# Performance work log

Measured on AMD Instinct MI355X. Metric: run time of the kernel, lower is better.

## Reference

```python
import jax, jax.numpy as jnp
import numpy as np

B, D, U = 8192, 1024, 1024


def setup_inputs() -> dict:
    key = jax.random.key(0)
    ks = jax.random.split(key, 11)
    scale = 0.05  # keras 'random_normal' initializer default stddev
    inp = {
        "inputs": jax.random.normal(ks[0], (B, D), jnp.float32),
        "h_tm1": jax.random.normal(ks[1], (B, U), jnp.float32),
        "c_tm1": jax.random.normal(ks[2], (B, U), jnp.float32),
        "W_i": jax.random.normal(ks[3], (D, U), jnp.float32) * scale,
        "U_i": jax.random.normal(ks[4], (U, U), jnp.float32) * scale,
        "b_i": jnp.zeros((U,), jnp.float32),
        "W_f": jax.random.normal(ks[5], (D, U), jnp.float32) * scale,
        "U_f": jax.random.normal(ks[6], (U, U), jnp.float32) * scale,
        "b_f": jnp.zeros((U,), jnp.float32),
        "W_c": jax.random.normal(ks[7], (D, U), jnp.float32) * scale,
        "U_c": jax.random.normal(ks[8], (U, U), jnp.float32) * scale,
        "b_c": jnp.zeros((U,), jnp.float32),
        "W_o": jax.random.normal(ks[9], (D, U), jnp.float32) * scale,
        "U_o": jax.random.normal(ks[10], (U, U), jnp.float32) * scale,
        "b_o": jnp.zeros((U,), jnp.float32),
    }
    return inp


def reference(inputs, h_tm1, c_tm1, W_i, U_i, b_i, W_f, U_f, b_f, W_c, U_c, b_c, W_o, U_o, b_o):
    # Concatenate the 4 gate projections into single GEMMs (same math, fused form)
    Wx = jnp.concatenate([W_i, W_f, W_c, W_o], axis=1)  # [D, 4U]
    Uh = jnp.concatenate([U_i, U_f, U_c, U_o], axis=1)  # [U, 4U]
    b = jnp.concatenate([b_i, b_f, b_c, b_o], axis=0)   # [4U]
    z = inputs @ Wx + h_tm1 @ Uh + b                     # [B, 4U]
    u = W_i.shape[1]
    zi, zf, zc, zo = z[:, :u], z[:, u:2 * u], z[:, 2 * u:3 * u], z[:, 3 * u:]
    i = jax.nn.sigmoid(zi)
    f = jax.nn.sigmoid(zf)
    c_ = jnp.tanh(zc)
    c = f * c_tm1 + i * c_
    o = jax.nn.sigmoid(zo)
    h = o * jnp.tanh(c)
    return (h, c)
```

## Files before the change

### kernel.cpp

```cpp
#include <hip/hip_runtime.h>
#include <hip/hip_bf16.h>
#include <cstdint>


using f32x4  = __attribute__((ext_vector_type(4))) float;
using short8 = __attribute__((ext_vector_type(8))) short;

__device__ __forceinline__ unsigned short f2bf(float f) {
  union { float f; unsigned int u; } v; v.f = f;
  unsigned int r = v.u + 0x7fffu + ((v.u >> 16) & 1u);
  return (unsigned short)(r >> 16);
}
__device__ __forceinline__ float sigmoidf_fast(float x) { return 1.f / (1.f + __expf(-x)); }
__device__ __forceinline__ float tanhf_fast(float x)    { return 1.f - 2.f / (__expf(2.f * x) + 1.f); }

__global__ void conv_a_kernel(const float* __restrict__ X, const float* __restrict__ H,
                              unsigned short* __restrict__ Abf) {
  int idx = blockIdx.x * blockDim.x + threadIdx.x;
  int b  = idx >> 8;
  int kq = (idx & 255) << 2;
  float4 x = *(const float4*)(X + (long)b * 1024 + kq);
  float4 h = *(const float4*)(H + (long)b * 1024 + kq);
  ushort4 xo, ho;
  xo.x = f2bf(x.x); xo.y = f2bf(x.y); xo.z = f2bf(x.z); xo.w = f2bf(x.w);
  ho.x = f2bf(h.x); ho.y = f2bf(h.y); ho.z = f2bf(h.z); ho.w = f2bf(h.w);
  *(ushort4*)(Abf + (long)b * 2048 + kq)        = xo;
  *(ushort4*)(Abf + (long)b * 2048 + 1024 + kq) = ho;
}

__global__ void conv_b_kernel(const float* W_i, const float* U_i,
                              const float* W_f, const float* U_f,
                              const float* W_c, const float* U_c,
                              const float* W_o, const float* U_o,
                              unsigned short* __restrict__ Bt) {
  __shared__ float tile[64][65];
  int z = blockIdx.z;
  const float* src;
  switch (z) {
    case 0: src = W_i; break; case 1: src = U_i; break;
    case 2: src = W_f; break; case 3: src = U_f; break;
    case 4: src = W_c; break; case 5: src = U_c; break;
    case 6: src = W_o; break; default: src = U_o; break;
  }
  int g = z >> 1, s = z & 1;
  int k0 = blockIdx.x * 64;
  int u0 = blockIdx.y * 64;
  int t = threadIdx.x;
  int c = t & 63, r0 = t >> 6;
#pragma unroll
  for (int i = 0; i < 16; ++i) {
    int r = i * 4 + r0;
    tile[r][c] = src[(long)(k0 + r) * 1024 + u0 + c];
  }
  __syncthreads();
  int ul = t >> 2;
  int ks = (t & 3) * 16;
  unsigned short outv[16];
#pragma unroll
  for (int j = 0; j < 16; ++j) outv[j] = f2bf(tile[ks + j][ul]);
  long n   = 4L * u0 + (ul >> 4) * 64 + g * 16 + (ul & 15);
  long col = (long)s * 1024 + k0 + ks;
  uint4* dst = (uint4*)(Bt + n * 2048 + col);
  dst[0] = *(uint4*)(outv);
  dst[1] = *(uint4*)(outv + 8);
}

__global__ __launch_bounds__(512, 2) void lstm_gemm_kernel(
    const unsigned short* __restrict__ Abf,
    const unsigned short* __restrict__ Btbf,
    const float* __restrict__ b_i, const float* __restrict__ b_f,
    const float* __restrict__ b_c, const float* __restrict__ b_o,
    const float* __restrict__ c_tm1,
    float* __restrict__ outH, float* __restrict__ outC) {
  __shared__ unsigned short smem[49152];

  int bid = blockIdx.x;
  int swz = (bid & 7) * 64 + (bid >> 3);
  int bm = swz >> 4;
  int bn = swz & 15;

  int t = threadIdx.x;
  int lane = t & 63;
  int w = t >> 6;
  int wm = w >> 2;
  int wn = w & 3;
  int rl = lane & 15;
  int kg = lane >> 4;

#define AOFFE(MI) ((wm * 128 + (MI) * 16 + rl) * 32 + \
    ((kg ^ (((wm * 128 + (MI) * 16 + rl) >> 1) & 3)) << 3))
#define BOFFE(NI) (8192 + (wn * 64 + (NI) * 16 + rl) * 32 + \
    ((kg ^ (((wn * 64 + (NI) * 16 + rl) >> 1) & 3)) << 3))
  const int offA0 = AOFFE(0), offA1 = AOFFE(1), offA2 = AOFFE(2), offA3 = AOFFE(3);
  const int offA4 = AOFFE(4), offA5 = AOFFE(5), offA6 = AOFFE(6), offA7 = AOFFE(7);
  const int offB0 = BOFFE(0), offB1 = BOFFE(1), offB2 = BOFFE(2), offB3 = BOFFE(3);
#undef AOFFE
#undef BOFFE

  int srow = t >> 2;
  int cbe  = (((t & 3) ^ ((srow >> 1) & 3))) << 3;
  const unsigned short* aS0 = Abf  + (long)(bm * 256 + srow) * 2048 + cbe;
  const unsigned short* aS1 = aS0 + 128L * 2048;
  const unsigned short* bS0 = Btbf + (long)(bn * 256 + srow) * 2048 + cbe;
  const unsigned short* bS1 = bS0 + 128L * 2048;
  const int dA = t * 8;

#define GLL(SRC, DELM)                                                                     \
  __builtin_amdgcn_global_load_lds((const __attribute__((address_space(1))) void*)(SRC),   \
      (__attribute__((address_space(3))) void*)(&smem[DELM]), 16, 0, 0)
#define VMC(N) asm volatile("s_waitcnt vmcnt(" #N ")" ::: "memory")

  f32x4 acc[8][4];
#pragma unroll
  for (int mi = 0; mi < 8; ++mi)
#pragma unroll
    for (int ni = 0; ni < 4; ++ni) acc[mi][ni] = (f32x4){0.f, 0.f, 0.f, 0.f};

  short8 aw0, aw1, aw2, aw3, bb0, bb1, bb2, bb3;

#define MF4(AF, MI)                                                                      \
  acc[MI][0] = __builtin_amdgcn_mfma_f32_16x16x32_bf16(AF, bb0, acc[MI][0], 0, 0, 0);    \
  acc[MI][1] = __builtin_amdgcn_mfma_f32_16x16x32_bf16(AF, bb1, acc[MI][1], 0, 0, 0);    \
  acc[MI][2] = __builtin_amdgcn_mfma_f32_16x16x32_bf16(AF, bb2, acc[MI][2], 0, 0, 0);    \
  acc[MI][3] = __builtin_amdgcn_mfma_f32_16x16x32_bf16(AF, bb3, acc[MI][3], 0, 0, 0);

#define WINDOW(RB, SB, KOFF, DOSTAGE, VMN, DOBAR)                              \
  {                                                                            \
    const unsigned short* Ab_ = smem + (RB) * 16384;                           \
    bb0 = *(const short8*)(Ab_ + offB0);                                       \
    bb1 = *(const short8*)(Ab_ + offB1);                                       \
    bb2 = *(const short8*)(Ab_ + offB2);                                       \
    bb3 = *(const short8*)(Ab_ + offB3);                                       \
    aw0 = *(const short8*)(Ab_ + offA0);                                       \
    aw1 = *(const short8*)(Ab_ + offA1);                                       \
    aw2 = *(const short8*)(Ab_ + offA2);                                       \
    aw3 = *(const short8*)(Ab_ + offA3);                                       \
    if (DOSTAGE) {                                                             \
      GLL(aS0 + (KOFF), (SB) * 16384 + dA);                                    \
      GLL(aS1 + (KOFF), (SB) * 16384 + 4096 + dA);                             \
    }                                                                          \
    __builtin_amdgcn_s_setprio(1);                                             \
    MF4(aw0, 0) MF4(aw1, 1) MF4(aw2, 2) MF4(aw3, 3)                            \
    __builtin_amdgcn_s_setprio(0);                                             \
    aw0 = *(const short8*)(Ab_ + offA4);                                       \
    aw1 = *(const short8*)(Ab_ + offA5);                                       \
    aw2 = *(const short8*)(Ab_ + offA6);                                       \
    aw3 = *(const short8*)(Ab_ + offA7);                                       \
    if (DOSTAGE) {                                                             \
      GLL(bS0 + (KOFF), (SB) * 16384 + 8192 + dA);                             \
      GLL(bS1 + (KOFF), (SB) * 16384 + 12288 + dA);                            \
    }                                                                          \
    __builtin_amdgcn_s_setprio(1);                                             \
    MF4(aw0, 4) MF4(aw1, 5) MF4(aw2, 6) MF4(aw3, 7)                            \
    __builtin_amdgcn_s_setprio(0);                                             \
    if ((VMN) == 4) VMC(4);                                                    \
    if ((VMN) == 0) VMC(0);                                                    \
    if (DOBAR) __builtin_amdgcn_s_barrier();                                   \
  }

  GLL(aS0, dA);            GLL(aS1, 4096 + dA);
  GLL(bS0, 8192 + dA);     GLL(bS1, 12288 + dA);
  GLL(aS0 + 32, 16384 + dA);        GLL(aS1 + 32, 16384 + 4096 + dA);
  GLL(bS0 + 32, 16384 + 8192 + dA); GLL(bS1 + 32, 16384 + 12288 + dA);
  VMC(4);
  __builtin_amdgcn_s_barrier();
  aS0 += 64; aS1 += 64; bS0 += 64; bS1 += 64;

  for (int g = 0; g < 20; ++g) {
    WINDOW(0, 2, 0,  1, 4, 1);
    WINDOW(1, 0, 32, 1, 4, 1);
    WINDOW(2, 1, 64, 1, 4, 1);
    aS0 += 96; aS1 += 96; bS0 += 96; bS1 += 96;
  }
  WINDOW(0, 2, 0,  1, 4, 1);
  WINDOW(1, 0, 32, 1, 4, 1);
  WINDOW(2, 0, 0,  0, 0, 1);
  WINDOW(0, 0, 0,  0, -1, 0);
#undef WINDOW
#undef MF4
#undef VMC
#undef GLL

  int mbase = bm * 256 + wm * 128;
  int nbase = bn * 256 + wn * 64;
  int u = (nbase >> 2) + rl;
  float bi_v = b_i[u], bf_v = b_f[u], bc_v = b_c[u], bo_v = b_o[u];
  int rquad = (lane >> 4) << 2;
#pragma unroll
  for (int mi = 0; mi < 8; ++mi) {
#pragma unroll
    for (int j = 0; j < 4; ++j) {
      int brow = mbase + mi * 16 + rquad + j;
      float zi = acc[mi][0][j] + bi_v;
      float zf = acc[mi][1][j] + bf_v;
      float zc = acc[mi][2][j] + bc_v;
      float zo = acc[mi][3][j] + bo_v;
      float ig = sigmoidf_fast(zi);
      float fg = sigmoidf_fast(zf);
      float cg = tanhf_fast(zc);
      float og = sigmoidf_fast(zo);
      float cp = c_tm1[(long)brow * 1024 + u];
      float cn = fg * cp + ig * cg;
      float hn = og * tanhf_fast(cn);
      outH[(long)brow * 1024 + u] = hn;
      outC[(long)brow * 1024 + u] = cn;
    }
  }
}

extern "C" void kernel_launch(void* const* d_in, const int* in_sizes, int n_in,
                              void* d_out, int out_size, void* d_ws, size_t ws_size,
                              hipStream_t stream) {
  (void)in_sizes; (void)n_in; (void)out_size; (void)ws_size;
  const float* X   = (const float*)d_in[0];
  const float* Hst = (const float*)d_in[1];
  const float* Cst = (const float*)d_in[2];
  const float* W_i = (const float*)d_in[3];
  const float* U_i = (const float*)d_in[4];
  const float* b_i = (const float*)d_in[5];
  const float* W_f = (const float*)d_in[6];
  const float* U_f = (const float*)d_in[7];
  const float* b_f = (const float*)d_in[8];
  const float* W_c = (const float*)d_in[9];
  const float* U_c = (const float*)d_in[10];
  const float* b_c = (const float*)d_in[11];
  const float* W_o = (const float*)d_in[12];
  const float* U_o = (const float*)d_in[13];
  const float* b_o = (const float*)d_in[14];

  unsigned short* Abf  = (unsigned short*)d_ws;
  unsigned short* Btbf = (unsigned short*)((char*)d_ws + 33554432);

  float* outH = (float*)d_out;
  float* outC = outH + 8192L * 1024;

  conv_a_kernel<<<8192, 256, 0, stream>>>(X, Hst, Abf);
  conv_b_kernel<<<dim3(16, 16, 8), 256, 0, stream>>>(W_i, U_i, W_f, U_f, W_c, U_c, W_o, U_o, Btbf);
  lstm_gemm_kernel<<<512, 512, 0, stream>>>(Abf, Btbf, b_i, b_f, b_c, b_o, Cst, outH, outC);
}
```

Baseline: 159.7 us.

## Load A fragments directly from global into registers, stage only B in LDS

After: 335.3 us. +109.9%, slower.

```diff
diff --git a/kernel.cpp b/kernel.cpp
--- a/kernel.cpp
+++ b/kernel.cpp
@@ -72,7 +72,7 @@
     const float* __restrict__ b_c, const float* __restrict__ b_o,
     const float* __restrict__ c_tm1,
     float* __restrict__ outH, float* __restrict__ outC) {
-  __shared__ unsigned short smem[49152];
+  __shared__ unsigned short smem[3 * 8192];
 
   int bid = blockIdx.x;
   int swz = (bid & 7) * 64 + (bid >> 3);
@@ -87,27 +87,27 @@
   int rl = lane & 15;
   int kg = lane >> 4;
 
-#define AOFFE(MI) ((wm * 128 + (MI) * 16 + rl) * 32 + \
-    ((kg ^ (((wm * 128 + (MI) * 16 + rl) >> 1) & 3)) << 3))
-#define BOFFE(NI) (8192 + (wn * 64 + (NI) * 16 + rl) * 32 + \
+#define BOFFE(NI) ((wn * 64 + (NI) * 16 + rl) * 32 + \
     ((kg ^ (((wn * 64 + (NI) * 16 + rl) >> 1) & 3)) << 3))
-  const int offA0 = AOFFE(0), offA1 = AOFFE(1), offA2 = AOFFE(2), offA3 = AOFFE(3);
-  const int offA4 = AOFFE(4), offA5 = AOFFE(5), offA6 = AOFFE(6), offA7 = AOFFE(7);
   const int offB0 = BOFFE(0), offB1 = BOFFE(1), offB2 = BOFFE(2), offB3 = BOFFE(3);
-#undef AOFFE
 #undef BOFFE
+
+  const unsigned short* gA = Abf + (long)(bm * 256 + wm * 128 + rl) * 2048 + kg * 8;
 
   int srow = t >> 2;
   int cbe  = (((t & 3) ^ ((srow >> 1) & 3))) << 3;
-  const unsigned short* aS0 = Abf  + (long)(bm * 256 + srow) * 2048 + cbe;
-  const unsigned short* aS1 = aS0 + 128L * 2048;
   const unsigned short* bS0 = Btbf + (long)(bn * 256 + srow) * 2048 + cbe;
   const unsigned short* bS1 = bS0 + 128L * 2048;
-  const int dA = t * 8;
+  const int dB = t * 8;
 
 #define GLL(SRC, DELM)                                                                     \
   __builtin_amdgcn_global_load_lds((const __attribute__((address_space(1))) void*)(SRC),   \
       (__attribute__((address_space(3))) void*)(&smem[DELM]), 16, 0, 0)
+#define GLLB(SB, KOFF)                                                         \
+  do {                                                                         \
+    GLL(bS0 + (KOFF), (SB) * 8192 + dB);                                       \
+    GLL(bS1 + (KOFF), (SB) * 8192 + 4096 + dB);                                \
+  } while (0)
 #define VMC(N) asm volatile("s_waitcnt vmcnt(" #N ")" ::: "memory")
 
   f32x4 acc[8][4];
@@ -116,7 +116,21 @@
 #pragma unroll
     for (int ni = 0; ni < 4; ++ni) acc[mi][ni] = (f32x4){0.f, 0.f, 0.f, 0.f};
 
-  short8 aw0, aw1, aw2, aw3, bb0, bb1, bb2, bb3;
+  short8 pa0, pa1, pa2, pa3, pa4, pa5, pa6, pa7;
+  short8 qa0, qa1, qa2, qa3, qa4, qa5, qa6, qa7;
+  short8 bb0, bb1, bb2, bb3;
+
+#define LOADA(S, KO)                                                           \
+  do {                                                                         \
+    S##a0 = *(const short8*)(gA + 0 * 32768 + (KO));                           \
+    S##a1 = *(const short8*)(gA + 1 * 32768 + (KO));                           \
+    S##a2 = *(const short8*)(gA + 2 * 32768 + (KO));                           \
+    S##a3 = *(const short8*)(gA + 3 * 32768 + (KO));                           \
+    S##a4 = *(const short8*)(gA + 4 * 32768 + (KO));                           \
+    S##a5 = *(const short8*)(gA + 5 * 32768 + (KO));                           \
+    S##a6 = *(const short8*)(gA + 6 * 32768 + (KO));                           \
+    S##a7 = *(const short8*)(gA + 7 * 32768 + (KO));                           \
+  } while (0)
 
 #define MF4(AF, MI)                                                                      \
   acc[MI][0] = __builtin_amdgcn_mfma_f32_16x16x32_bf16(AF, bb0, acc[MI][0], 0, 0, 0);    \
@@ -124,61 +138,48 @@
   acc[MI][2] = __builtin_amdgcn_mfma_f32_16x16x32_bf16(AF, bb2, acc[MI][2], 0, 0, 0);    \
   acc[MI][3] = __builtin_amdgcn_mfma_f32_16x16x32_bf16(AF, bb3, acc[MI][3], 0, 0, 0);
 
-#define WINDOW(RB, SB, KOFF, DOSTAGE, VMN, DOBAR)                              \
+#define WINDOW(RB, SB, KOA, KOB, C, N, DOA, DOST, VMN, DOBAR)                  \
   {                                                                            \
-    const unsigned short* Ab_ = smem + (RB) * 16384;                           \
-    bb0 = *(const short8*)(Ab_ + offB0);                                       \
-    bb1 = *(const short8*)(Ab_ + offB1);                                       \
-    bb2 = *(const short8*)(Ab_ + offB2);                                       \
-    bb3 = *(const short8*)(Ab_ + offB3);                                       \
-    aw0 = *(const short8*)(Ab_ + offA0);                                       \
-    aw1 = *(const short8*)(Ab_ + offA1);                                       \
-    aw2 = *(const short8*)(Ab_ + offA2);                                       \
-    aw3 = *(const short8*)(Ab_ + offA3);                                       \
-    if (DOSTAGE) {                                                             \
-      GLL(aS0 + (KOFF), (SB) * 16384 + dA);                                    \
-      GLL(aS1 + (KOFF), (SB) * 16384 + 4096 + dA);                             \
-    }                                                                          \
+    if (DOA) LOADA(N, KOA);                                                    \
+    const unsigned short* Bb_ = smem + (RB) * 8192;                            \
+    bb0 = *(const short8*)(Bb_ + offB0);                                       \
+    bb1 = *(const short8*)(Bb_ + offB1);                                       \
+    bb2 = *(const short8*)(Bb_ + offB2);                                       \
+    bb3 = *(const short8*)(Bb_ + offB3);                                       \
+    if (DOST) GLLB(SB, KOB);                                                   \
     __builtin_amdgcn_s_setprio(1);                                             \
-    MF4(aw0, 0) MF4(aw1, 1) MF4(aw2, 2) MF4(aw3, 3)                            \
+    MF4(C##a0, 0) MF4(C##a1, 1) MF4(C##a2, 2) MF4(C##a3, 3)                    \
+    MF4(C##a4, 4) MF4(C##a5, 5) MF4(C##a6, 6) MF4(C##a7, 7)                    \
     __builtin_amdgcn_s_setprio(0);                                             \
-    aw0 = *(const short8*)(Ab_ + offA4);                                       \
-    aw1 = *(const short8*)(Ab_ + offA5);                                       \
-    aw2 = *(const short8*)(Ab_ + offA6);                                       \
-    aw3 = *(const short8*)(Ab_ + offA7);                                       \
-    if (DOSTAGE) {                                                             \
-      GLL(bS0 + (KOFF), (SB) * 16384 + 8192 + dA);                             \
-      GLL(bS1 + (KOFF), (SB) * 16384 + 12288 + dA);                            \
-    }                                                                          \
-    __builtin_amdgcn_s_setprio(1);                                             \
-    MF4(aw0, 4) MF4(aw1, 5) MF4(aw2, 6) MF4(aw3, 7)                            \
-    __builtin_amdgcn_s_setprio(0);                                             \
-    if ((VMN) == 4) VMC(4);                                                    \
+    if ((VMN) == 2) VMC(2);                                                    \
     if ((VMN) == 0) VMC(0);                                                    \
     if (DOBAR) __builtin_amdgcn_s_barrier();                                   \
   }
 
-  GLL(aS0, dA);            GLL(aS1, 4096 + dA);
-  GLL(bS0, 8192 + dA);     GLL(bS1, 12288 + dA);
-  GLL(aS0 + 32, 16384 + dA);        GLL(aS1 + 32, 16384 + 4096 + dA);
-  GLL(bS0 + 32, 16384 + 8192 + dA); GLL(bS1 + 32, 16384 + 12288 + dA);
-  VMC(4);
+  GLLB(0, 0);
+  GLLB(1, 32);
+  LOADA(p, 0);
+  VMC(10);
   __builtin_amdgcn_s_barrier();
-  aS0 += 64; aS1 += 64; bS0 += 64; bS1 += 64;
-
-  for (int g = 0; g < 20; ++g) {
-    WINDOW(0, 2, 0,  1, 4, 1);
-    WINDOW(1, 0, 32, 1, 4, 1);
-    WINDOW(2, 1, 64, 1, 4, 1);
-    aS0 += 96; aS1 += 96; bS0 += 96; bS1 += 96;
-  }
-  WINDOW(0, 2, 0,  1, 4, 1);
-  WINDOW(1, 0, 32, 1, 4, 1);
-  WINDOW(2, 0, 0,  0, 0, 1);
-  WINDOW(0, 0, 0,  0, -1, 0);
+
+  for (int g = 0; g < 10; ++g) {
+    WINDOW(0, 2, 32,  64,  p, q, 1, 1, 2, 1);
+    WINDOW(1, 0, 64,  96,  q, p, 1, 1, 2, 1);
+    WINDOW(2, 1, 96,  128, p, q, 1, 1, 2, 1);
+    WINDOW(0, 2, 128, 160, q, p, 1, 1, 2, 1);
+    WINDOW(1, 0, 160, 192, p, q, 1, 1, 2, 1);
+    WINDOW(2, 1, 192, 224, q, p, 1, 1, 2, 1);
+    gA += 192; bS0 += 192; bS1 += 192;
+  }
+  WINDOW(0, 2, 32, 64, p, q, 1, 1, 2, 1);
+  WINDOW(1, 0, 64, 96, q, p, 1, 1, 2, 1);
+  WINDOW(2, 0, 96, 0,  p, q, 1, 0, 0, 1);
+  WINDOW(0, 0, 0,  0,  q, p, 0, 0, -1, 0);
 #undef WINDOW
 #undef MF4
+#undef LOADA
 #undef VMC
+#undef GLLB
 #undef GLL
 
   int mbase = bm * 256 + wm * 128;
```

## Shrink GEMM block tile to 256x128 and raise occupancy to four blocks per CU

Applied to the files above, without the earlier changes.

Result: slower. 174.3 us (+9.1%).

```diff
diff --git a/kernel.cpp b/kernel.cpp
--- a/kernel.cpp
+++ b/kernel.cpp
@@ -65,54 +65,58 @@
   dst[1] = *(uint4*)(outv + 8);
 }
 
-__global__ __launch_bounds__(512, 2) void lstm_gemm_kernel(
+__global__ __launch_bounds__(512, 4) void lstm_gemm_kernel(
     const unsigned short* __restrict__ Abf,
     const unsigned short* __restrict__ Btbf,
     const float* __restrict__ b_i, const float* __restrict__ b_f,
     const float* __restrict__ b_c, const float* __restrict__ b_o,
     const float* __restrict__ c_tm1,
     float* __restrict__ outH, float* __restrict__ outC) {
-  __shared__ unsigned short smem[49152];
+  __shared__ unsigned short smem[3 * 12288];
 
   int bid = blockIdx.x;
-  int swz = (bid & 7) * 64 + (bid >> 3);
-  int bm = swz >> 4;
-  int bn = swz & 15;
+  int swz = (bid & 7) * 128 + (bid >> 3);
+  int bm = swz >> 5;
+  int bn = swz & 31;
 
   int t = threadIdx.x;
   int lane = t & 63;
   int w = t >> 6;
-  int wm = w >> 2;
-  int wn = w & 3;
+  int wm = w >> 1;
+  int wn = w & 1;
   int rl = lane & 15;
   int kg = lane >> 4;
 
-#define AOFFE(MI) ((wm * 128 + (MI) * 16 + rl) * 32 + \
-    ((kg ^ (((wm * 128 + (MI) * 16 + rl) >> 1) & 3)) << 3))
-#define BOFFE(NI) (8192 + (wn * 64 + (NI) * 16 + rl) * 32 + \
+#define AOFFE(MI) (((wm * 64 + (MI) * 16 + rl) * 32) + \
+    ((kg ^ (((wm * 64 + (MI) * 16 + rl) >> 1) & 3)) << 3))
+#define BOFFE(NI) (8192 + ((wn * 64 + (NI) * 16 + rl) * 32) + \
     ((kg ^ (((wn * 64 + (NI) * 16 + rl) >> 1) & 3)) << 3))
   const int offA0 = AOFFE(0), offA1 = AOFFE(1), offA2 = AOFFE(2), offA3 = AOFFE(3);
-  const int offA4 = AOFFE(4), offA5 = AOFFE(5), offA6 = AOFFE(6), offA7 = AOFFE(7);
   const int offB0 = BOFFE(0), offB1 = BOFFE(1), offB2 = BOFFE(2), offB3 = BOFFE(3);
 #undef AOFFE
 #undef BOFFE
 
   int srow = t >> 2;
-  int cbe  = (((t & 3) ^ ((srow >> 1) & 3))) << 3;
+  int cbe  = ((t & 3) ^ ((srow >> 1) & 3)) << 3;
   const unsigned short* aS0 = Abf  + (long)(bm * 256 + srow) * 2048 + cbe;
   const unsigned short* aS1 = aS0 + 128L * 2048;
-  const unsigned short* bS0 = Btbf + (long)(bn * 256 + srow) * 2048 + cbe;
-  const unsigned short* bS1 = bS0 + 128L * 2048;
+  const unsigned short* bS0 = Btbf + (long)(bn * 128 + srow) * 2048 + cbe;
   const int dA = t * 8;
 
 #define GLL(SRC, DELM)                                                                     \
   __builtin_amdgcn_global_load_lds((const __attribute__((address_space(1))) void*)(SRC),   \
       (__attribute__((address_space(3))) void*)(&smem[DELM]), 16, 0, 0)
+#define STAGE(SB, KOFF)                                                        \
+  do {                                                                         \
+    GLL(aS0 + (KOFF), (SB) * 12288 + dA);                                      \
+    GLL(aS1 + (KOFF), (SB) * 12288 + 4096 + dA);                               \
+    GLL(bS0 + (KOFF), (SB) * 12288 + 8192 + dA);                               \
+  } while (0)
 #define VMC(N) asm volatile("s_waitcnt vmcnt(" #N ")" ::: "memory")
 
-  f32x4 acc[8][4];
-#pragma unroll
-  for (int mi = 0; mi < 8; ++mi)
+  f32x4 acc[4][4];
+#pragma unroll
+  for (int mi = 0; mi < 4; ++mi)
 #pragma unroll
     for (int ni = 0; ni < 4; ++ni) acc[mi][ni] = (f32x4){0.f, 0.f, 0.f, 0.f};
 
@@ -126,68 +130,53 @@
 
 #define WINDOW(RB, SB, KOFF, DOSTAGE, VMN, DOBAR)                              \
   {                                                                            \
-    const unsigned short* Ab_ = smem + (RB) * 16384;                           \
-    bb0 = *(const short8*)(Ab_ + offB0);                                       \
-    bb1 = *(const short8*)(Ab_ + offB1);                                       \
-    bb2 = *(const short8*)(Ab_ + offB2);                                       \
-    bb3 = *(const short8*)(Ab_ + offB3);                                       \
-    aw0 = *(const short8*)(Ab_ + offA0);                                       \
-    aw1 = *(const short8*)(Ab_ + offA1);                                       \
-    aw2 = *(const short8*)(Ab_ + offA2);                                       \
-    aw3 = *(const short8*)(Ab_ + offA3);                                       \
-    if (DOSTAGE) {                                                             \
-      GLL(aS0 + (KOFF), (SB) * 16384 + dA);                                    \
-      GLL(aS1 + (KOFF), (SB) * 16384 + 4096 + dA);                             \
-    }                                                                          \
+    const unsigned short* S_ = smem + (RB) * 12288;                            \
+    bb0 = *(const short8*)(S_ + offB0);                                        \
+    bb1 = *(const short8*)(S_ + offB1);                                        \
+    bb2 = *(const short8*)(S_ + offB2);                                        \
+    bb3 = *(const short8*)(S_ + offB3);                                        \
+    aw0 = *(const short8*)(S_ + offA0);                                        \
+    aw1 = *(const short8*)(S_ + offA1);                                        \
+    aw2 = *(const short8*)(S_ + offA2);                                        \
+    aw3 = *(const short8*)(S_ + offA3);                                        \
+    if (DOSTAGE) STAGE(SB, KOFF);                                              \
     __builtin_amdgcn_s_setprio(1);                                             \
     MF4(aw0, 0) MF4(aw1, 1) MF4(aw2, 2) MF4(aw3, 3)                            \
     __builtin_amdgcn_s_setprio(0);                                             \
-    aw0 = *(const short8*)(Ab_ + offA4);                                       \
-    aw1 = *(const short8*)(Ab_ + offA5);                                       \
-    aw2 = *(const short8*)(Ab_ + offA6);                                       \
-    aw3 = *(const short8*)(Ab_ + offA7);                                       \
-    if (DOSTAGE) {                                                             \
-      GLL(bS0 + (KOFF), (SB) * 16384 + 8192 + dA);                             \
-      GLL(bS1 + (KOFF), (SB) * 16384 + 12288 + dA);                            \
-    }                                                                          \
-    __builtin_amdgcn_s_setprio(1);                                             \
-    MF4(aw0, 4) MF4(aw1, 5) MF4(aw2, 6) MF4(aw3, 7)                            \
-    __builtin_amdgcn_s_setprio(0);                                             \
-    if ((VMN) == 4) VMC(4);                                                    \
+    if ((VMN) == 3) VMC(3);                                                    \
     if ((VMN) == 0) VMC(0);                                                    \
     if (DOBAR) __builtin_amdgcn_s_barrier();                                   \
   }
 
-  GLL(aS0, dA);            GLL(aS1, 4096 + dA);
-  GLL(bS0, 8192 + dA);     GLL(bS1, 12288 + dA);
-  GLL(aS0 + 32, 16384 + dA);        GLL(aS1 + 32, 16384 + 4096 + dA);
-  GLL(bS0 + 32, 16384 + 8192 + dA); GLL(bS1 + 32, 16384 + 12288 + dA);
-  VMC(4);
+  STAGE(0, 0);
+  STAGE(1, 32);
+  VMC(3);
   __builtin_amdgcn_s_barrier();
-  aS0 += 64; aS1 += 64; bS0 += 64; bS1 += 64;
+  aS0 += 64; aS1 += 64; bS0 += 64;
 
   for (int g = 0; g < 20; ++g) {
-    WINDOW(0, 2, 0,  1, 4, 1);
-    WINDOW(1, 0, 32, 1, 4, 1);
-    WINDOW(2, 1, 64, 1, 4, 1);
-    aS0 += 96; aS1 += 96; bS0 += 96; bS1 += 96;
-  }
-  WINDOW(0, 2, 0,  1, 4, 1);
-  WINDOW(1, 0, 32, 1, 4, 1);
+    WINDOW(0, 2, 0,  1, 3, 1);
+    WINDOW(1, 0, 32, 1, 3, 1);
+    WINDOW(2, 1, 64, 1, 3, 1);
+    aS0 += 96; aS1 += 96; bS0 += 96;
+  }
+  WINDOW(0, 2, 0,  1, 3, 1);
+  WINDOW(1, 0, 32, 1, 3, 1);
   WINDOW(2, 0, 0,  0, 0, 1);
   WINDOW(0, 0, 0,  0, -1, 0);
 #undef WINDOW
 #undef MF4
 #undef VMC
+#undef STAGE
 #undef GLL
 
-  int mbase = bm * 256 + wm * 128;
-  int nbase = bn * 256 + wn * 64;
+  int mbase = bm * 256 + wm * 64;
+  int nbase = bn * 128 + wn * 64;
   int u = (nbase >> 2) + rl;
   float bi_v = b_i[u], bf_v = b_f[u], bc_v = b_c[u], bo_v = b_o[u];
   int rquad = (lane >> 4) << 2;
 #pragma unroll
-  for (int mi = 0; mi < 8; ++mi) {
+  for (int mi = 0; mi < 4; ++mi) {
 #pragma unroll
     for (int j = 0; j < 4; ++j) {
       int brow = mbase + mi * 16 + rquad + j;
@@ -236,5 +225,5 @@
 
   conv_a_kernel<<<8192, 256, 0, stream>>>(X, Hst, Abf);
   conv_b_kernel<<<dim3(16, 16, 8), 256, 0, stream>>>(W_i, U_i, W_f, U_f, W_c, U_c, W_o, U_o, Btbf);
-  lstm_gemm_kernel<<<512, 512, 0, stream>>>(Abf, Btbf, b_i, b_f, b_c, b_o, Cst, outH, outC);
-}
+  lstm_gemm_kernel<<<1024, 512, 0, stream>>>(Abf, Btbf, b_i, b_f, b_c, b_o, Cst, outH, outC);
+}
```

## Switch GEMM to 32x32x16 MFMA with reshaped warp tiling

Applied to the files above, without the earlier changes.

New measurement: 168.9 us. 1.06x slower.

```diff
diff --git a/kernel.cpp b/kernel.cpp
--- a/kernel.cpp
+++ b/kernel.cpp
@@ -3,7 +3,7 @@
 #include <cstdint>
 
 
-using f32x4  = __attribute__((ext_vector_type(4))) float;
+using f32x16 = __attribute__((ext_vector_type(16))) float;
 using short8 = __attribute__((ext_vector_type(8))) short;
 
 __device__ __forceinline__ unsigned short f2bf(float f) {
@@ -58,7 +58,7 @@
   unsigned short outv[16];
 #pragma unroll
   for (int j = 0; j < 16; ++j) outv[j] = f2bf(tile[ks + j][ul]);
-  long n   = 4L * u0 + (ul >> 4) * 64 + g * 16 + (ul & 15);
+  long n   = 4L * u0 + (ul >> 5) * 128 + g * 32 + (ul & 31);
   long col = (long)s * 1024 + k0 + ks;
   uint4* dst = (uint4*)(Bt + n * 2048 + col);
   dst[0] = *(uint4*)(outv);
@@ -82,23 +82,24 @@
   int t = threadIdx.x;
   int lane = t & 63;
   int w = t >> 6;
-  int wm = w >> 2;
-  int wn = w & 3;
-  int rl = lane & 15;
-  int kg = lane >> 4;
-
-#define AOFFE(MI) ((wm * 128 + (MI) * 16 + rl) * 32 + \
-    ((kg ^ (((wm * 128 + (MI) * 16 + rl) >> 1) & 3)) << 3))
-#define BOFFE(NI) (8192 + (wn * 64 + (NI) * 16 + rl) * 32 + \
-    ((kg ^ (((wn * 64 + (NI) * 16 + rl) >> 1) & 3)) << 3))
-  const int offA0 = AOFFE(0), offA1 = AOFFE(1), offA2 = AOFFE(2), offA3 = AOFFE(3);
-  const int offA4 = AOFFE(4), offA5 = AOFFE(5), offA6 = AOFFE(6), offA7 = AOFFE(7);
-  const int offB0 = BOFFE(0), offB1 = BOFFE(1), offB2 = BOFFE(2), offB3 = BOFFE(3);
+  int wm = w >> 1;
+  int wn = w & 1;
+  int rl = lane & 31;
+  int kh = lane >> 5;
+
+#define AOFFE(MI, KK) (((wm * 64 + (MI) * 32 + rl) * 32) + \
+    ((((kh) + (KK) * 2) ^ (((wm * 64 + (MI) * 32 + rl) >> 1) & 3)) << 3))
+#define BOFFE(NI, KK) (8192 + ((wn * 128 + (NI) * 32 + rl) * 32) + \
+    ((((kh) + (KK) * 2) ^ (((wn * 128 + (NI) * 32 + rl) >> 1) & 3)) << 3))
+  const int offA00 = AOFFE(0, 0), offA10 = AOFFE(1, 0);
+  const int offA01 = AOFFE(0, 1), offA11 = AOFFE(1, 1);
+  const int offB00 = BOFFE(0, 0), offB10 = BOFFE(1, 0), offB20 = BOFFE(2, 0), offB30 = BOFFE(3, 0);
+  const int offB01 = BOFFE(0, 1), offB11 = BOFFE(1, 1), offB21 = BOFFE(2, 1), offB31 = BOFFE(3, 1);
 #undef AOFFE
 #undef BOFFE
 
   int srow = t >> 2;
-  int cbe  = (((t & 3) ^ ((srow >> 1) & 3))) << 3;
+  int cbe  = ((t & 3) ^ ((srow >> 1) & 3)) << 3;
   const unsigned short* aS0 = Abf  + (long)(bm * 256 + srow) * 2048 + cbe;
   const unsigned short* aS1 = aS0 + 128L * 2048;
   const unsigned short* bS0 = Btbf + (long)(bn * 256 + srow) * 2048 + cbe;
@@ -110,48 +111,61 @@
       (__attribute__((address_space(3))) void*)(&smem[DELM]), 16, 0, 0)
 #define VMC(N) asm volatile("s_waitcnt vmcnt(" #N ")" ::: "memory")
 
-  f32x4 acc[8][4];
-#pragma unroll
-  for (int mi = 0; mi < 8; ++mi)
-#pragma unroll
-    for (int ni = 0; ni < 4; ++ni) acc[mi][ni] = (f32x4){0.f, 0.f, 0.f, 0.f};
-
-  short8 aw0, aw1, aw2, aw3, bb0, bb1, bb2, bb3;
-
-#define MF4(AF, MI)                                                                      \
-  acc[MI][0] = __builtin_amdgcn_mfma_f32_16x16x32_bf16(AF, bb0, acc[MI][0], 0, 0, 0);    \
-  acc[MI][1] = __builtin_amdgcn_mfma_f32_16x16x32_bf16(AF, bb1, acc[MI][1], 0, 0, 0);    \
-  acc[MI][2] = __builtin_amdgcn_mfma_f32_16x16x32_bf16(AF, bb2, acc[MI][2], 0, 0, 0);    \
-  acc[MI][3] = __builtin_amdgcn_mfma_f32_16x16x32_bf16(AF, bb3, acc[MI][3], 0, 0, 0);
+  f32x16 acc[2][4];
+#pragma unroll
+  for (int mi = 0; mi < 2; ++mi)
+#pragma unroll
+    for (int ni = 0; ni < 4; ++ni)
+#pragma unroll
+      for (int j = 0; j < 16; ++j) acc[mi][ni][j] = 0.f;
+
+  short8 a00, a10, a01, a11;
+  short8 b00, b10, b20, b30, b01, b11, b21, b31;
+
+#define MFMA32(A, B, C) __builtin_amdgcn_mfma_f32_32x32x16_bf16(A, B, C, 0, 0, 0)
 
 #define WINDOW(RB, SB, KOFF, DOSTAGE, VMN, DOBAR)                              \
   {                                                                            \
-    const unsigned short* Ab_ = smem + (RB) * 16384;                           \
-    bb0 = *(const short8*)(Ab_ + offB0);                                       \
-    bb1 = *(const short8*)(Ab_ + offB1);                                       \
-    bb2 = *(const short8*)(Ab_ + offB2);                                       \
-    bb3 = *(const short8*)(Ab_ + offB3);                                       \
-    aw0 = *(const short8*)(Ab_ + offA0);                                       \
-    aw1 = *(const short8*)(Ab_ + offA1);                                       \
-    aw2 = *(const short8*)(Ab_ + offA2);                                       \
-    aw3 = *(const short8*)(Ab_ + offA3);                                       \
+    const unsigned short* S_ = smem + (RB) * 16384;                            \
+    b00 = *(const short8*)(S_ + offB00);                                       \
+    b10 = *(const short8*)(S_ + offB10);                                       \
+    b20 = *(const short8*)(S_ + offB20);                                       \
+    b30 = *(const short8*)(S_ + offB30);                                       \
+    a00 = *(const short8*)(S_ + offA00);                                       \
+    a10 = *(const short8*)(S_ + offA10);                                       \
     if (DOSTAGE) {                                                             \
       GLL(aS0 + (KOFF), (SB) * 16384 + dA);                                    \
       GLL(aS1 + (KOFF), (SB) * 16384 + 4096 + dA);                             \
     }                                                                          \
     __builtin_amdgcn_s_setprio(1);                                             \
-    MF4(aw0, 0) MF4(aw1, 1) MF4(aw2, 2) MF4(aw3, 3)                            \
+    acc[0][0] = MFMA32(a00, b00, acc[0][0]);                                   \
+    acc[0][1] = MFMA32(a00, b10, acc[0][1]);                                   \
+    acc[0][2] = MFMA32(a00, b20, acc[0][2]);                                   \
+    acc[0][3] = MFMA32(a00, b30, acc[0][3]);                                   \
+    acc[1][0] = MFMA32(a10, b00, acc[1][0]);                                   \
+    acc[1][1] = MFMA32(a10, b10, acc[1][1]);                                   \
+    acc[1][2] = MFMA32(a10, b20, acc[1][2]);                                   \
+    acc[1][3] = MFMA32(a10, b30, acc[1][3]);                                   \
     __builtin_amdgcn_s_setprio(0);                                             \
-    aw0 = *(const short8*)(Ab_ + offA4);                                       \
-    aw1 = *(const short8*)(Ab_ + offA5);                                       \
-    aw2 = *(const short8*)(Ab_ + offA6);                                       \
-    aw3 = *(const short8*)(Ab_ + offA7);                                       \
+    b01 = *(const short8*)(S_ + offB01);                                       \
+    b11 = *(const short8*)(S_ + offB11);                                       \
+    b21 = *(const short8*)(S_ + offB21);                                       \
+    b31 = *(const short8*)(S_ + offB31);                                       \
+    a01 = *(const short8*)(S_ + offA01);                                       \
+    a11 = *(const short8*)(S_ + offA11);                                       \
     if (DOSTAGE) {                                                             \
       GLL(bS0 + (KOFF), (SB) * 16384 + 8192 + dA);                             \
       GLL(bS1 + (KOFF), (SB) * 16384 + 12288 + dA);                            \
     }                                                                          \
     __builtin_amdgcn_s_setprio(1);                                             \
-    MF4(aw0, 4) MF4(aw1, 5) MF4(aw2, 6) MF4(aw3, 7)                            \
+    acc[0][0] = MFMA32(a01, b01, acc[0][0]);                                   \
+    acc[0][1] = MFMA32(a01, b11, acc[0][1]);                                   \
+    acc[0][2] = MFMA32(a01, b21, acc[0][2]);                                   \
+    acc[0][3] = MFMA32(a01, b31, acc[0][3]);                                   \
+    acc[1][0] = MFMA32(a11, b01, acc[1][0]);                                   \
+    acc[1][1] = MFMA32(a11, b11, acc[1][1]);                                   \
+    acc[1][2] = MFMA32(a11, b21, acc[1][2]);                                   \
+    acc[1][3] = MFMA32(a11, b31, acc[1][3]);                                   \
     __builtin_amdgcn_s_setprio(0);                                             \
     if ((VMN) == 4) VMC(4);                                                    \
     if ((VMN) == 0) VMC(0);                                                    \
@@ -177,20 +191,19 @@
   WINDOW(2, 0, 0,  0, 0, 1);
   WINDOW(0, 0, 0,  0, -1, 0);
 #undef WINDOW
-#undef MF4
+#undef MFMA32
 #undef VMC
 #undef GLL
 
-  int mbase = bm * 256 + wm * 128;
-  int nbase = bn * 256 + wn * 64;
+  int mbase = bm * 256 + wm * 64;
+  int nbase = bn * 256 + wn * 128;
   int u = (nbase >> 2) + rl;
   float bi_v = b_i[u], bf_v = b_f[u], bc_v = b_c[u], bo_v = b_o[u];
-  int rquad = (lane >> 4) << 2;
-#pragma unroll
-  for (int mi = 0; mi < 8; ++mi) {
-#pragma unroll
-    for (int j = 0; j < 4; ++j) {
-      int brow = mbase + mi * 16 + rquad + j;
+#pragma unroll
+  for (int mi = 0; mi < 2; ++mi) {
+#pragma unroll
+    for (int j = 0; j < 16; ++j) {
+      int brow = mbase + mi * 32 + (j & 3) + 8 * (j >> 2) + 4 * kh;
       float zi = acc[mi][0][j] + bi_v;
       float zf = acc[mi][1][j] + bf_v;
       float zc = acc[mi][2][j] + bc_v;
```
